# Performance work log

Hardware: AMD Instinct MI355X
Metric: run time of the kernel (lower is better)

## Reference

```python
import jax, jax.numpy as jnp
import numpy as np
from jax import lax

D_MODEL = 1024
KERNEL = 7
EPS = 1e-8


def setup_inputs() -> dict:
    key = jax.random.key(0)
    ks = jax.random.split(key, 8)
    B, T, D = 4, 4096, D_MODEL
    x = jax.random.normal(ks[0], (B, T, D), dtype=jnp.float32)
    # rotary tables [T, D/2]
    pos = jnp.arange(T, dtype=jnp.float32)[:, None]
    inv_freq = 1.0 / (10000.0 ** (jnp.arange(D // 2, dtype=jnp.float32) / (D // 2)))
    ang = pos * inv_freq[None, :]
    sin = jnp.sin(ang)
    cos = jnp.cos(ang)
    # params
    W_proj = jax.random.normal(ks[1], (D, 2 * D), dtype=jnp.float32) * (1.0 / np.sqrt(D))
    b_proj = jnp.zeros((2 * D,), dtype=jnp.float32)
    dw_kernel = jax.random.normal(ks[2], (KERNEL, 1, D), dtype=jnp.float32) * 0.1  # [K,1,C] WIO depthwise
    dw_bias = jnp.zeros((D,), dtype=jnp.float32)
    gamma = jnp.ones((D,), dtype=jnp.float32)
    return {"x": x, "sin": sin, "cos": cos, "W_proj": W_proj, "b_proj": b_proj,
            "dw_kernel": dw_kernel, "dw_bias": dw_bias, "gamma": gamma}


def reference(x, sin, cos, W_proj, b_proj, dw_kernel, dw_bias, gamma):
    D = D_MODEL
    proj = jnp.einsum('btd,df->btf', x, W_proj) + b_proj          # [B,T,2D]
    x_a, x_b = proj[..., :D], proj[..., D:]
    # interleaved rotary: even/odd pairs
    x1 = x_a[..., 0::2]                                            # [B,T,D/2]
    x2 = x_a[..., 1::2]
    c = cos[None, :, :]
    s = sin[None, :, :]
    r1 = x1 * c - x2 * s
    r2 = x1 * s + x2 * c
    x_rot = jnp.stack([r1, r2], axis=-1).reshape(x_a.shape)        # re-interleave
    # depthwise conv1d, SAME padding
    conv = lax.conv_general_dilated(
        x_rot, dw_kernel, window_strides=(1,), padding='SAME',
        dimension_numbers=('NWC', 'WIO', 'NWC'), feature_group_count=D) + dw_bias
    act = conv * jax.nn.sigmoid(conv)                              # swish
    gated = act * jax.nn.sigmoid(x_b)
    rms = jnp.sqrt(jnp.mean(jnp.square(gated), axis=-1, keepdims=True) + EPS)
    return gamma * (gated / rms)
```

## Files before the change

### kernel.cpp

```cpp
#include <hip/hip_runtime.h>
#include <stdint.h>

#define D_MODEL 1024
#define T_LEN   4096
#define B_SZ    4
#define NROWS   (B_SZ * T_LEN)
#define NPROJ   (2 * D_MODEL)
#define CHUNK   16

#define BM 256
#define BN 256
#define BK 64
#define NT (D_MODEL / BK)

typedef __attribute__((ext_vector_type(8))) __bf16 bf16x8;
typedef __attribute__((ext_vector_type(4))) float  f32x4;

using as1_void = __attribute__((address_space(1))) void;
using as3_void = __attribute__((address_space(3))) void;

__device__ inline float bf2f(unsigned short u) {
    union { unsigned int i; float f; } v; v.i = ((unsigned int)u) << 16; return v.f;
}
__device__ inline unsigned short f2bf(float f) {
    union { float f; unsigned int i; } v; v.f = f;
    return (unsigned short)((v.i + 0x7fffu + ((v.i >> 16) & 1u)) >> 16);
}
__device__ inline float sigmoidf(float x) { return 1.0f / (1.0f + __expf(-x)); }

__global__ __launch_bounds__(256) void k_cvt(const float* __restrict__ x,
                                             unsigned short* __restrict__ xb,
                                             const float* __restrict__ W,
                                             unsigned short* __restrict__ wt) {
    __shared__ unsigned short tile[32][33];
    int bid = blockIdx.x;
    if (bid < (NROWS * D_MODEL) / (256 * 4)) {
        int i = (bid * 256 + threadIdx.x) * 4;
        float4 v = *reinterpret_cast<const float4*>(x + i);
        ushort4 o;
        o.x = f2bf(v.x); o.y = f2bf(v.y); o.z = f2bf(v.z); o.w = f2bf(v.w);
        *reinterpret_cast<ushort4*>(xb + i) = o;
    } else {
        bid -= (NROWS * D_MODEL) / (256 * 4);
        int n0 = (bid & 63) * 32, k0 = (bid >> 6) * 32;
        int c = threadIdx.x & 31, r = threadIdx.x >> 5;
        #pragma unroll
        for (int i = 0; i < 4; i++) {
            int kk = r + i * 8;
            tile[kk][c] = f2bf(W[(uint64_t)(k0 + kk) * NPROJ + n0 + c]);
        }
        __syncthreads();
        #pragma unroll
        for (int i = 0; i < 4; i++) {
            int nn = r + i * 8;
            wt[(uint64_t)(n0 + nn) * D_MODEL + k0 + c] = tile[c][nn];
        }
    }
}

__global__ __launch_bounds__(512, 2) void k_gemm(const unsigned short* __restrict__ xb,
                                                 const unsigned short* __restrict__ wt,
                                                 const float* __restrict__ bias,
                                                 const float* __restrict__ sinp,
                                                 const float* __restrict__ cosp,
                                                 unsigned short* __restrict__ projb) {
    __shared__ __align__(16) unsigned short As[2 * BM * BK];
    __shared__ __align__(16) unsigned short Bs[2 * BM * BK];

    const int tid  = threadIdx.x;
    const int lane = tid & 63;
    const int w    = tid >> 6;
    const int wm   = w >> 2;
    const int wn   = w & 3;

    const int bid = blockIdx.x;
    const int wg  = (bid & 7) * 64 + (bid >> 3);
    const int n0  = (wg >> 6) * BN;
    const int m0  = (wg & 63) * BM;

    const int srow = tid >> 3;
    const int scol = ((tid & 7) ^ (srow & 7)) * 8;
    const int fr   = lane & 15;
    const int fq   = lane >> 4;

    f32x4 acc[8][4] = {};

    auto STAGE = [&](int buf, int ks) {
        #pragma unroll
        for (int i = 0; i < 4; ++i) {
            const unsigned short* ga = xb + (uint64_t)(m0 + i * 64 + srow) * D_MODEL + ks + scol;
            __builtin_amdgcn_global_load_lds((as1_void*)(void*)ga,
                (as3_void*)(void*)&As[buf * (BM * BK) + i * 4096 + w * 512], 16, 0, 0);
        }
        #pragma unroll
        for (int i = 0; i < 4; ++i) {
            const unsigned short* gb = wt + (uint64_t)(n0 + i * 64 + srow) * D_MODEL + ks + scol;
            __builtin_amdgcn_global_load_lds((as1_void*)(void*)gb,
                (as3_void*)(void*)&Bs[buf * (BM * BK) + i * 4096 + w * 512], 16, 0, 0);
        }
    };

    STAGE(0, 0);
    __syncthreads();

    for (int t = 0; t < NT; ++t) {
        const int cur = t & 1;
        if (t + 1 < NT) STAGE(1 - cur, (t + 1) * BK);

        const unsigned short* Ab = &As[cur * (BM * BK)];
        const unsigned short* Bb = &Bs[cur * (BM * BK)];
        #pragma unroll
        for (int kk = 0; kk < BK; kk += 32) {
            const int slot = (kk >> 3) + fq;
            bf16x8 b[4];
            #pragma unroll
            for (int n = 0; n < 4; n++) {
                const int rb = wn * 64 + n * 16 + fr;
                b[n] = *reinterpret_cast<const bf16x8*>(&Bb[rb * 64 + ((slot ^ (fr & 7)) * 8)]);
            }
            #pragma unroll
            for (int m = 0; m < 8; m++) {
                const int ra = wm * 128 + m * 16 + fr;
                bf16x8 a = *reinterpret_cast<const bf16x8*>(&Ab[ra * 64 + ((slot ^ (fr & 7)) * 8)]);
                #pragma unroll
                for (int n = 0; n < 4; n++)
                    acc[m][n] = __builtin_amdgcn_mfma_f32_16x16x32_bf16(a, b[n], acc[m][n], 0, 0, 0);
            }
        }
        __syncthreads();
    }

    if (n0 < D_MODEL) {
        #pragma unroll
        for (int m = 0; m < 8; m++) {
            const int grow = m0 + wm * 128 + m * 16 + fq * 4;
            #pragma unroll
            for (int n = 0; n < 4; n++) {
                const int gcol = n0 + wn * 64 + n * 16 + fr;
                const float bv = bias[gcol];
                const int pidx = gcol >> 1;
                const bool evn = (gcol & 1) == 0;
                #pragma unroll
                for (int r = 0; r < 4; r++) {
                    const int trow = (grow + r) & (T_LEN - 1);
                    float v = acc[m][n][r] + bv;
                    float other = __shfl_xor(v, 1);
                    float cv = cosp[(uint64_t)trow * (D_MODEL / 2) + pidx];
                    float sv = sinp[(uint64_t)trow * (D_MODEL / 2) + pidx];
                    float ro = evn ? (v * cv - other * sv) : (other * sv + v * cv);
                    projb[(uint64_t)(grow + r) * NPROJ + gcol] = f2bf(ro);
                }
            }
        }
    } else {
        #pragma unroll
        for (int m = 0; m < 8; m++) {
            const int grow = m0 + wm * 128 + m * 16 + fq * 4;
            #pragma unroll
            for (int n = 0; n < 4; n++) {
                const int gcol = n0 + wn * 64 + n * 16 + fr;
                const float bv = bias[gcol];
                #pragma unroll
                for (int r = 0; r < 4; r++) {
                    projb[(uint64_t)(grow + r) * NPROJ + gcol] = f2bf(sigmoidf(acc[m][n][r] + bv));
                }
            }
        }
    }
}

__global__ __launch_bounds__(512) void k_post(const unsigned short* __restrict__ projb,
                                              const float* __restrict__ kw,
                                              const float* __restrict__ dwb,
                                              const float* __restrict__ gamma,
                                              float* __restrict__ out) {
    const int blk  = blockIdx.x;
    const int b    = blk / (T_LEN / CHUNK);
    const int t0   = (blk % (T_LEN / CHUNK)) * CHUNK;
    const int c    = threadIdx.x;
    const int d0   = c * 2;
    const uint64_t bbase = (uint64_t)b * T_LEN;

    float kwv[7][2];
    #pragma unroll
    for (int j = 0; j < 7; j++) {
        kwv[j][0] = kw[j * D_MODEL + d0];
        kwv[j][1] = kw[j * D_MODEL + d0 + 1];
    }
    const float bv0 = dwb[d0], bv1 = dwb[d0 + 1];
    const float gm0 = gamma[d0], gm1 = gamma[d0 + 1];

    __shared__ float red[2][8];

    auto load_row = [&](int tj, float& o0, float& o1) {
        if ((unsigned)tj < (unsigned)T_LEN) {
            ushort2 u = *reinterpret_cast<const ushort2*>(projb + (bbase + tj) * NPROJ + d0);
            o0 = bf2f(u.x); o1 = bf2f(u.y);
        } else { o0 = 0.f; o1 = 0.f; }
    };

    float rg[6][2];
    #pragma unroll
    for (int j = 0; j < 6; j++) load_row(t0 - 3 + j, rg[j][0], rg[j][1]);
    float nx0, nx1;
    load_row(t0 + 3, nx0, nx1);

    ushort2 xb_cur = *reinterpret_cast<const ushort2*>(projb + (bbase + t0) * NPROJ + D_MODEL + d0);

    for (int t = t0; t < t0 + CHUNK; ++t) {
        const float r60 = nx0, r61 = nx1;

        float acc0 = rg[0][0] * kwv[0][0] + rg[1][0] * kwv[1][0] + rg[2][0] * kwv[2][0]
                   + rg[3][0] * kwv[3][0] + rg[4][0] * kwv[4][0] + rg[5][0] * kwv[5][0]
                   + r60 * kwv[6][0] + bv0;
        float acc1 = rg[0][1] * kwv[0][1] + rg[1][1] * kwv[1][1] + rg[2][1] * kwv[2][1]
                   + rg[3][1] * kwv[3][1] + rg[4][1] * kwv[4][1] + rg[5][1] * kwv[5][1]
                   + r61 * kwv[6][1] + bv1;

        load_row(t + 4, nx0, nx1);
        const ushort2 xb_use = xb_cur;
        if (t + 1 < t0 + CHUNK) {
            xb_cur = *reinterpret_cast<const ushort2*>(projb + (bbase + t + 1) * NPROJ + D_MODEL + d0);
        }

        float a0 = acc0 * sigmoidf(acc0);
        float a1 = acc1 * sigmoidf(acc1);
        float g0 = a0 * bf2f(xb_use.x);
        float g1 = a1 * bf2f(xb_use.y);

        float ssq = g0 * g0 + g1 * g1;
        #pragma unroll
        for (int off = 32; off; off >>= 1) ssq += __shfl_down(ssq, off);
        const int p = t & 1;
        if ((threadIdx.x & 63) == 0) red[p][threadIdx.x >> 6] = ssq;
        __syncthreads();
        float total = red[p][0] + red[p][1] + red[p][2] + red[p][3]
                    + red[p][4] + red[p][5] + red[p][6] + red[p][7];
        const float inv = 1.0f / sqrtf(total * (1.0f / (float)D_MODEL) + 1e-8f);

        float2 o;
        o.x = g0 * inv * gm0;
        o.y = g1 * inv * gm1;
        *reinterpret_cast<float2*>(out + (bbase + t) * D_MODEL + d0) = o;

        #pragma unroll
        for (int j = 0; j < 5; j++) { rg[j][0] = rg[j + 1][0]; rg[j][1] = rg[j + 1][1]; }
        rg[5][0] = r60; rg[5][1] = r61;
    }
}

extern "C" void kernel_launch(void* const* d_in, const int* in_sizes, int n_in,
                              void* d_out, int out_size, void* d_ws, size_t ws_size,
                              hipStream_t stream) {
    const float* x     = (const float*)d_in[0];
    const float* sinp  = (const float*)d_in[1];
    const float* cosp  = (const float*)d_in[2];
    const float* W     = (const float*)d_in[3];
    const float* bproj = (const float*)d_in[4];
    const float* dwk   = (const float*)d_in[5];
    const float* dwb   = (const float*)d_in[6];
    const float* gamma = (const float*)d_in[7];
    float* out = (float*)d_out;

    unsigned short* xb    = (unsigned short*)d_ws;
    unsigned short* wt    = xb + (size_t)NROWS * D_MODEL;
    unsigned short* projb = wt + (size_t)NPROJ * D_MODEL;

    const int cvt_x_blocks = (NROWS * D_MODEL) / (256 * 4);
    const int cvt_w_blocks = (NPROJ / 32) * (D_MODEL / 32);
    k_cvt<<<cvt_x_blocks + cvt_w_blocks, 256, 0, stream>>>(x, xb, W, wt);
    k_gemm<<<(NPROJ / BN) * (NROWS / BM), 512, 0, stream>>>(xb, wt, bproj, sinp, cosp, projb);
    k_post<<<B_SZ * (T_LEN / CHUNK), 512, 0, stream>>>(projb, dwk, dwb, gamma, out);
}
```

Baseline: 152.1 us.

## Split rotary epilogue out of GEMM into vectorized k_rope kernel; move sigmoid to post

Removes the rotary and sigmoid epilogues from the GEMM so every tile stores plain bias-added bf16. A new vectorized k_rope kernel rewrites the first half of each projected row in place, reading sin/cos as float4. The gate sigmoid moves into k_post, and k_post's CHUNK doubles. This trades the GEMM's scattered per-element sin/cos loads and shuffles for an extra kernel launch and another full pass over the x_a half of projb, and it rounds x_a to bf16 before rotation rather than after.

```diff
diff --git a/kernel.cpp b/kernel.cpp
--- a/kernel.cpp
+++ b/kernel.cpp
@@ -6,7 +6,7 @@
 #define B_SZ    4
 #define NROWS   (B_SZ * T_LEN)
 #define NPROJ   (2 * D_MODEL)
-#define CHUNK   16
+#define CHUNK   32
 
 #define BM 256
 #define BN 256
@@ -61,8 +61,6 @@
 __global__ __launch_bounds__(512, 2) void k_gemm(const unsigned short* __restrict__ xb,
                                                  const unsigned short* __restrict__ wt,
                                                  const float* __restrict__ bias,
-                                                 const float* __restrict__ sinp,
-                                                 const float* __restrict__ cosp,
                                                  unsigned short* __restrict__ projb) {
     __shared__ __align__(16) unsigned short As[2 * BM * BK];
     __shared__ __align__(16) unsigned short Bs[2 * BM * BK];
@@ -130,43 +128,47 @@
         __syncthreads();
     }
 
-    if (n0 < D_MODEL) {
-        #pragma unroll
-        for (int m = 0; m < 8; m++) {
-            const int grow = m0 + wm * 128 + m * 16 + fq * 4;
+    #pragma unroll
+    for (int m = 0; m < 8; m++) {
+        const int grow = m0 + wm * 128 + m * 16 + fq * 4;
+        #pragma unroll
+        for (int n = 0; n < 4; n++) {
+            const int gcol = n0 + wn * 64 + n * 16 + fr;
+            const float bv = bias[gcol];
             #pragma unroll
-            for (int n = 0; n < 4; n++) {
-                const int gcol = n0 + wn * 64 + n * 16 + fr;
-                const float bv = bias[gcol];
-                const int pidx = gcol >> 1;
-                const bool evn = (gcol & 1) == 0;
-                #pragma unroll
-                for (int r = 0; r < 4; r++) {
-                    const int trow = (grow + r) & (T_LEN - 1);
-                    float v = acc[m][n][r] + bv;
-                    float other = __shfl_xor(v, 1);
-                    float cv = cosp[(uint64_t)trow * (D_MODEL / 2) + pidx];
-                    float sv = sinp[(uint64_t)trow * (D_MODEL / 2) + pidx];
-                    float ro = evn ? (v * cv - other * sv) : (other * sv + v * cv);
-                    projb[(uint64_t)(grow + r) * NPROJ + gcol] = f2bf(ro);
-                }
+            for (int r = 0; r < 4; r++) {
+                projb[(uint64_t)(grow + r) * NPROJ + gcol] = f2bf(acc[m][n][r] + bv);
             }
         }
-    } else {
-        #pragma unroll
-        for (int m = 0; m < 8; m++) {
-            const int grow = m0 + wm * 128 + m * 16 + fq * 4;
-            #pragma unroll
-            for (int n = 0; n < 4; n++) {
-                const int gcol = n0 + wn * 64 + n * 16 + fr;
-                const float bv = bias[gcol];
-                #pragma unroll
-                for (int r = 0; r < 4; r++) {
-                    projb[(uint64_t)(grow + r) * NPROJ + gcol] = f2bf(sigmoidf(acc[m][n][r] + bv));
-                }
-            }
-        }
-    }
+    }
+}
+
+__global__ __launch_bounds__(256) void k_rope(unsigned short* __restrict__ projb,
+                                              const float* __restrict__ sinp,
+                                              const float* __restrict__ cosp) {
+    const uint64_t u  = (uint64_t)blockIdx.x * 256 + threadIdx.x;
+    const int row = (int)(u >> 7);
+    const int c0  = ((int)u & 127) * 4;
+    const int t   = row & (T_LEN - 1);
+
+    unsigned int* p = reinterpret_cast<unsigned int*>(projb + (uint64_t)row * NPROJ + c0 * 2);
+    uint4  v  = *reinterpret_cast<const uint4*>(p);
+    float4 cc = *reinterpret_cast<const float4*>(cosp + (uint64_t)t * (D_MODEL / 2) + c0);
+    float4 ss = *reinterpret_cast<const float4*>(sinp + (uint64_t)t * (D_MODEL / 2) + c0);
+
+    auto rot = [&](unsigned int w, float cv, float sv) -> unsigned int {
+        float x0 = bf2f((unsigned short)(w & 0xffffu));
+        float x1 = bf2f((unsigned short)(w >> 16));
+        float r0 = x0 * cv - x1 * sv;
+        float r1 = x0 * sv + x1 * cv;
+        return (unsigned int)f2bf(r0) | ((unsigned int)f2bf(r1) << 16);
+    };
+    uint4 o;
+    o.x = rot(v.x, cc.x, ss.x);
+    o.y = rot(v.y, cc.y, ss.y);
+    o.z = rot(v.z, cc.z, ss.z);
+    o.w = rot(v.w, cc.w, ss.w);
+    *reinterpret_cast<uint4*>(p) = o;
 }
 
 __global__ __launch_bounds__(512) void k_post(const unsigned short* __restrict__ projb,
@@ -225,8 +227,8 @@
 
         float a0 = acc0 * sigmoidf(acc0);
         float a1 = acc1 * sigmoidf(acc1);
-        float g0 = a0 * bf2f(xb_use.x);
-        float g1 = a1 * bf2f(xb_use.y);
+        float g0 = a0 * sigmoidf(bf2f(xb_use.x));
+        float g1 = a1 * sigmoidf(bf2f(xb_use.y));
 
         float ssq = g0 * g0 + g1 * g1;
         #pragma unroll
@@ -269,6 +271,7 @@
     const int cvt_x_blocks = (NROWS * D_MODEL) / (256 * 4);
     const int cvt_w_blocks = (NPROJ / 32) * (D_MODEL / 32);
     k_cvt<<<cvt_x_blocks + cvt_w_blocks, 256, 0, stream>>>(x, xb, W, wt);
-    k_gemm<<<(NPROJ / BN) * (NROWS / BM), 512, 0, stream>>>(xb, wt, bproj, sinp, cosp, projb);
+    k_gemm<<<(NPROJ / BN) * (NROWS / BM), 512, 0, stream>>>(xb, wt, bproj, projb);
+    k_rope<<<(NROWS * 128) / 256, 256, 0, stream>>>(projb, sinp, cosp);
     k_post<<<B_SZ * (T_LEN / CHUNK), 512, 0, stream>>>(projb, dwk, dwb, gamma, out);
 }
```

Result: slower. 164.0 us (+7.9%).
